# Optimization experiments

Hardware: AMD Instinct MI355X
Metric: run time of the kernel (lower is better)

The kernel has to match this reference:

```python
import jax, jax.numpy as jnp
import numpy as np

B, F, V, E = 16384, 39, 100000, 16
D0, D1, D2 = 32, 32, 32

def setup_inputs() -> dict:
    key = jax.random.key(0)
    ks = jax.random.split(key, 12)
    return {
        "Xi": jax.random.randint(ks[0], (B, F, 1), 0, V),
        "Xv": jax.random.uniform(ks[1], (B, F), dtype=jnp.float32),
        "emb_tables": jax.random.normal(ks[2], (F, V, E), dtype=jnp.float32),
        "w_first": jax.random.normal(ks[3], (D0, F, E), dtype=jnp.float32),
        "w_inner": jax.random.normal(ks[4], (D0, F, E), dtype=jnp.float32),
        "lin1_W": jax.random.normal(ks[5], (D1, D0), dtype=jnp.float32) * 0.1,
        "lin1_b": jax.random.normal(ks[6], (D1,), dtype=jnp.float32) * 0.1,
        "lin2_W": jax.random.normal(ks[7], (D2, D1), dtype=jnp.float32) * 0.1,
        "lin2_b": jax.random.normal(ks[8], (D2,), dtype=jnp.float32) * 0.1,
        "last_W": jax.random.normal(ks[9], (1, D2), dtype=jnp.float32) * 0.1,
        "last_b": jax.random.normal(ks[10], (1,), dtype=jnp.float32) * 0.1,
    }

def reference(Xi, Xv, emb_tables, w_first, w_inner, lin1_W, lin1_b, lin2_W, lin2_b, last_W, last_b):
    idx = Xi[:, :, 0]                                  # [B,F]
    # per-field embedding gather, scaled by feature value
    emb = emb_tables[jnp.arange(F)[None, :], idx]      # [B,F,E]
    emb = emb * Xv[:, :, None]                         # [B,F,E]
    # first-order: nested loops over (D0, F) collapse to one einsum
    first = jnp.einsum('bfe,dfe->bd', emb, w_first)    # [B,D0]
    # inner-product second-order: (sum over fields of <emb_f, w_df>)^2
    s = jnp.einsum('bfe,dfe->bd', emb, w_inner)        # [B,D0]
    x = first + s * s
    # deep MLP (relu, no dropout/batchnorm in inference)
    x = jax.nn.relu(x @ lin1_W.T + lin1_b)
    x = jax.nn.relu(x @ lin2_W.T + lin2_b)
    x = x @ last_W.T + last_b                          # [B,1]
    return jnp.sum(x, axis=1)                          # [B]
```

## Files before the change

### kernel.cpp

```cpp
#include <hip/hip_runtime.h>


namespace {

typedef _Float16 half8 __attribute__((ext_vector_type(8)));
typedef _Float16 half4 __attribute__((ext_vector_type(4)));
typedef float floatx4 __attribute__((ext_vector_type(4)));
typedef float f32x4 __attribute__((ext_vector_type(4)));

constexpr int Bn = 16384;
constexpr int Fn = 39;
constexpr int Vn = 100000;
constexpr int En = 16;
constexpr int M = 32;
constexpr int KST = 20;
constexpr int GITER = 10;
constexpr int NTOT = Bn * Fn;

constexpr int CHUNK_LOG = 11;
constexpr int CHUNK = 1 << CHUNK_LOG;
constexpr int NB = (Vn + CHUNK - 1) / CHUNK;
constexpr int NBUCKET = Fn * NB;
constexpr int CAP = 512;
constexpr int CUR_STRIDE = 16;

constexpr size_t OFF_CUR = 0;
constexpr size_t OFF_ENT = 131072;
constexpr size_t OFF_AEMB = 8388608;

__device__ __forceinline__ half8 cvt8(float4 a, float4 b) {
    half8 h;
    h[0] = (_Float16)a.x; h[1] = (_Float16)a.y;
    h[2] = (_Float16)a.z; h[3] = (_Float16)a.w;
    h[4] = (_Float16)b.x; h[5] = (_Float16)b.y;
    h[6] = (_Float16)b.z; h[7] = (_Float16)b.w;
    return h;
}

__device__ __forceinline__ half4 cvt4(f32x4 a) {
    half4 h;
    h[0] = (_Float16)a[0];
    h[1] = (_Float16)a[1];
    h[2] = (_Float16)a[2];
    h[3] = (_Float16)a[3];
    return h;
}

__global__ __launch_bounds__(256) void pnn_zero(unsigned int* __restrict__ cur)
{
    const int i = blockIdx.x * 256 + threadIdx.x;
    if (i < NBUCKET) cur[(size_t)i * CUR_STRIDE] = 0u;
}

__global__ __launch_bounds__(256) void pnn_bin(
    const int* __restrict__ Xi,
    const float* __restrict__ Xv,
    unsigned int* __restrict__ cur,
    uint2* __restrict__ ent)
{
    const int i = blockIdx.x * 256 + threadIdx.x;
    if (i >= NTOT) return;
    const unsigned int idx = (unsigned int)Xi[i];
    const float v = Xv[i];
    const unsigned int b = (unsigned int)i / (unsigned int)Fn;
    const unsigned int f = (unsigned int)i - b * (unsigned int)Fn;
    const unsigned int bucket = f * NB + (idx >> CHUNK_LOG);
    const unsigned int pos = atomicAdd(&cur[(size_t)bucket * CUR_STRIDE], 1u);
    if (pos < CAP) {
        uint2 e;
        e.x = b | ((idx & (unsigned int)(CHUNK - 1)) << 14);
        e.y = __float_as_uint(v);
        ent[(size_t)bucket * CAP + pos] = e;
    }
}

__global__ __launch_bounds__(256) void pnn_scatter(
    const float* __restrict__ T,
    const unsigned int* __restrict__ cur,
    const uint2* __restrict__ ent,
    float* __restrict__ Aemb)
{
    const int blk = blockIdx.x;
    const int f = blk / NB;
    const int ch = blk - f * NB;
    const int tid = threadIdx.x;

    unsigned int cnt = cur[(size_t)blk * CUR_STRIDE];
    if (cnt > CAP) cnt = CAP;
    const int ntask = (int)cnt * 4;

    const float* __restrict__ Tb =
        T + ((size_t)f * Vn + (size_t)ch * CHUNK) * En;
    const uint2* __restrict__ eb = ent + (size_t)blk * CAP;

    for (int g = 0; g < 2; ++g) {
        f32x4 v[4]; float s[4]; int c4[4]; unsigned int bb[4]; bool ok[4];
#pragma unroll
        for (int k = 0; k < 4; ++k) {
            const int task = tid + (g * 4 + k) * 256;
            ok[k] = task < ntask;
            if (ok[k]) {
                const uint2 e = eb[task >> 2];
                const int c = task & 3;
                bb[k] = e.x & 16383u;
                const unsigned int il = e.x >> 14;
                s[k] = __uint_as_float(e.y);
                c4[k] = c;
                v[k] = *reinterpret_cast<const f32x4*>(
                    Tb + (size_t)il * En + c * 4);
            }
        }
#pragma unroll
        for (int k = 0; k < 4; ++k) {
            if (ok[k]) {
                f32x4 r;
                r[0] = v[k][0] * s[k];
                r[1] = v[k][1] * s[k];
                r[2] = v[k][2] * s[k];
                r[3] = v[k][3] * s[k];
                *reinterpret_cast<f32x4*>(
                    Aemb + ((size_t)bb[k] * Fn + f) * En + c4[k] * 4) = r;
            }
        }
    }
}

struct SMemGather {
    _Float16 At[2][KST * 512];
};
struct SMemMlp {
    float x[M * 69];
    float wsh[2176];
    float r1[1024];
    float r2[1024];
};
union SMemU {
    SMemGather g;
    SMemMlp m;
};

__global__ __launch_bounds__(512, 4) void pnn_gemm(
    const float* __restrict__ Aemb,
    const float* __restrict__ w_first,
    const float* __restrict__ w_inner,
    const float* __restrict__ lin1_W,
    const float* __restrict__ lin1_b,
    const float* __restrict__ lin2_W,
    const float* __restrict__ lin2_b,
    const float* __restrict__ last_W,
    const float* __restrict__ last_b,
    float* __restrict__ out)
{
    __shared__ SMemU sm;

    const int tid = threadIdx.x;
    const int lane = tid & 63;
    const int wv = tid >> 6;
    const int q = wv & 1;
    const int t16 = wv >> 1;
    const int row0 = blockIdx.x * M;

    if (tid < 64) {
        half8 z = {0, 0, 0, 0, 0, 0, 0, 0};
        const int qq = tid >> 5;
        *reinterpret_cast<half8*>(
            &sm.g.At[qq][((KST - 1) * 64 + 32 + (tid & 31)) * 8]) = z;
    }

    f32x4 v[GITER];
    int   slot[GITER];
    bool  ok[GITER];
#pragma unroll
    for (int it = 0; it < GITER; ++it) {
        const int i = tid + it * 512;
        ok[it] = (i < M * Fn * 4);
        if (ok[it]) {
            const int j = i >> 2, c = i & 3;
            const int r = j & 31, f = j >> 5;
            v[it] = *reinterpret_cast<const f32x4*>(
                Aemb + ((size_t)(row0 + r) * Fn + f) * En + c * 4);
            slot[it] = (r >> 4) * (KST * 512)
                     + (((f >> 1) * 64) + (f & 1) * 32 + (r & 15)) * 8
                     + (c >> 1) * 128 + (c & 1) * 4;
        }
    }
#pragma unroll
    for (int it = 0; it < GITER; ++it) {
        if (ok[it])
            *reinterpret_cast<half4*>(&sm.g.At[0][0] + slot[it]) = cvt4(v[it]);
    }
    __syncthreads();

    const int n = t16 * 16 + (lane & 15);
    const int kq = lane >> 4;
    const float* wrow = (n < 32) ? (w_first + (size_t)n * 624)
                                 : (w_inner + (size_t)(n - 32) * 624);
    const _Float16* aLds = &sm.g.At[q][lane * 8];

    floatx4 acc = {0.0f, 0.0f, 0.0f, 0.0f};
#pragma unroll
    for (int t = 0; t < KST; ++t) {
        const half8 af = *reinterpret_cast<const half8*>(aLds + t * 512);
        half8 bf;
        if (t == KST - 1 && kq >= 2) {
            bf = half8{0, 0, 0, 0, 0, 0, 0, 0};
        } else {
            const int kb = t * 32 + kq * 8;
            const float4 a = *reinterpret_cast<const float4*>(wrow + kb);
            const float4 b = *reinterpret_cast<const float4*>(wrow + kb + 4);
            bf = cvt8(a, b);
        }
        acc = __builtin_amdgcn_mfma_f32_16x16x32_f16(af, bf, acc, 0, 0, 0);
    }

    __syncthreads();

    {
        const int col = t16 * 16 + (lane & 15);
        const int rbase = q * 16 + (lane >> 4) * 4;
#pragma unroll
        for (int r = 0; r < 4; ++r)
            sm.m.x[(rbase + r) * 69 + col] = acc[r];
    }

    for (int i = tid; i < 2145; i += 512) {
        float vv;
        if (i < 1024)      vv = lin1_W[i];
        else if (i < 2048) vv = lin2_W[i - 1024];
        else if (i < 2080) vv = lin1_b[i - 2048];
        else if (i < 2112) vv = lin2_b[i - 2080];
        else if (i < 2144) vv = last_W[i - 2112];
        else               vv = last_b[0];
        sm.m.wsh[i] = vv;
    }
    __syncthreads();

    for (int p = tid; p < 1024; p += 512) {
        const int j = p >> 5, r = p & 31;
        const float fi = sm.m.x[r * 69 + j];
        const float sq = sm.m.x[r * 69 + 32 + j];
        sm.m.r1[j * 32 + r] = fi + sq * sq;
    }
    __syncthreads();

    {
        const int r = tid & 31, n0 = (tid >> 5) * 2;
        float a0 = sm.m.wsh[2048 + n0];
        float a1 = sm.m.wsh[2048 + n0 + 1];
#pragma unroll
        for (int j = 0; j < 32; ++j) {
            const float xj = sm.m.r1[j * 32 + r];
            a0 = fmaf(sm.m.wsh[n0 * 32 + j],       xj, a0);
            a1 = fmaf(sm.m.wsh[(n0 + 1) * 32 + j], xj, a1);
        }
        sm.m.r2[n0 * 32 + r]       = fmaxf(a0, 0.0f);
        sm.m.r2[(n0 + 1) * 32 + r] = fmaxf(a1, 0.0f);
    }
    __syncthreads();

    {
        const int r = tid & 31, n0 = (tid >> 5) * 2;
        float a0 = sm.m.wsh[2080 + n0];
        float a1 = sm.m.wsh[2080 + n0 + 1];
#pragma unroll
        for (int j = 0; j < 32; ++j) {
            const float xj = sm.m.r2[j * 32 + r];
            a0 = fmaf(sm.m.wsh[1024 + n0 * 32 + j],       xj, a0);
            a1 = fmaf(sm.m.wsh[1024 + (n0 + 1) * 32 + j], xj, a1);
        }
        sm.m.r1[n0 * 32 + r]       = fmaxf(a0, 0.0f);
        sm.m.r1[(n0 + 1) * 32 + r] = fmaxf(a1, 0.0f);
    }
    __syncthreads();

    if (tid < M) {
        float res = sm.m.wsh[2144];
#pragma unroll
        for (int j = 0; j < 32; ++j)
            res = fmaf(sm.m.wsh[2112 + j], sm.m.r1[j * 32 + tid], res);
        out[row0 + tid] = res;
    }
}

}

extern "C" void kernel_launch(void* const* d_in, const int* in_sizes, int n_in,
                              void* d_out, int out_size, void* d_ws, size_t ws_size,
                              hipStream_t stream) {
    (void)in_sizes; (void)n_in; (void)out_size; (void)ws_size;
    const int*   Xi      = (const int*)d_in[0];
    const float* Xv      = (const float*)d_in[1];
    const float* T       = (const float*)d_in[2];
    const float* w_first = (const float*)d_in[3];
    const float* w_inner = (const float*)d_in[4];
    const float* lin1_W  = (const float*)d_in[5];
    const float* lin1_b  = (const float*)d_in[6];
    const float* lin2_W  = (const float*)d_in[7];
    const float* lin2_b  = (const float*)d_in[8];
    const float* last_W  = (const float*)d_in[9];
    const float* last_b  = (const float*)d_in[10];
    float* out = (float*)d_out;

    unsigned int* cur = (unsigned int*)((char*)d_ws + OFF_CUR);
    uint2*        ent = (uint2*)((char*)d_ws + OFF_ENT);
    float*        Aemb = (float*)((char*)d_ws + OFF_AEMB);

    hipLaunchKernelGGL(pnn_zero, dim3((NBUCKET + 255) / 256), dim3(256), 0, stream,
                       cur);
    hipLaunchKernelGGL(pnn_bin, dim3((NTOT + 255) / 256), dim3(256), 0, stream,
                       Xi, Xv, cur, ent);
    hipLaunchKernelGGL(pnn_scatter, dim3(NBUCKET), dim3(256), 0, stream,
                       T, cur, ent, Aemb);
    hipLaunchKernelGGL(pnn_gemm, dim3(Bn / M), dim3(512), 0, stream,
                       Aemb, w_first, w_inner,
                       lin1_W, lin1_b, lin2_W, lin2_b, last_W, last_b, out);
}
```

Baseline: 385.7 us.

## Stage each embedding table chunk in LDS before scaling selected rows

The scatter kernel becomes a select kernel with 512 threads. Each block first copies its whole 1024-row slice of the embedding table into shared memory with coalesced loads. It then serves every binned lookup from shared memory, scales it by the feature value and writes it to Aemb. The bucket chunk size is halved and the per-bucket capacity and workspace offsets change to match. The aim is to replace scattered 64-byte global gathers with streaming reads, but every block now reads the full chunk (the entire table overall) even though only a small fraction of rows is used, which greatly increases the bytes read.

```diff
diff --git a/kernel.cpp b/kernel.cpp
--- a/kernel.cpp
+++ b/kernel.cpp
@@ -17,16 +17,16 @@
 constexpr int GITER = 10;
 constexpr int NTOT = Bn * Fn;
 
-constexpr int CHUNK_LOG = 11;
+constexpr int CHUNK_LOG = 10;
 constexpr int CHUNK = 1 << CHUNK_LOG;
 constexpr int NB = (Vn + CHUNK - 1) / CHUNK;
 constexpr int NBUCKET = Fn * NB;
-constexpr int CAP = 512;
+constexpr int CAP = 320;
 constexpr int CUR_STRIDE = 16;
 
 constexpr size_t OFF_CUR = 0;
-constexpr size_t OFF_ENT = 131072;
-constexpr size_t OFF_AEMB = 8388608;
+constexpr size_t OFF_ENT = 262144;
+constexpr size_t OFF_AEMB = 16777216;
 
 __device__ __forceinline__ half8 cvt8(float4 a, float4 b) {
     half8 h;
@@ -74,54 +74,45 @@
     }
 }
 
-__global__ __launch_bounds__(256) void pnn_scatter(
+__global__ __launch_bounds__(512) void pnn_select(
     const float* __restrict__ T,
     const unsigned int* __restrict__ cur,
     const uint2* __restrict__ ent,
     float* __restrict__ Aemb)
 {
+    __shared__ float Lw[CHUNK * En];
     const int blk = blockIdx.x;
     const int f = blk / NB;
     const int ch = blk - f * NB;
     const int tid = threadIdx.x;
 
+    const int rows = min(CHUNK, Vn - ch * CHUNK);
+    const f32x4* __restrict__ T4 = reinterpret_cast<const f32x4*>(
+        T + ((size_t)f * Vn + (size_t)ch * CHUNK) * En);
+    f32x4* L4 = reinterpret_cast<f32x4*>(Lw);
+    const int nchunk = rows * 4;
+    for (int i = tid; i < nchunk; i += 512)
+        L4[i] = T4[i];
+    __syncthreads();
+
     unsigned int cnt = cur[(size_t)blk * CUR_STRIDE];
     if (cnt > CAP) cnt = CAP;
     const int ntask = (int)cnt * 4;
-
-    const float* __restrict__ Tb =
-        T + ((size_t)f * Vn + (size_t)ch * CHUNK) * En;
     const uint2* __restrict__ eb = ent + (size_t)blk * CAP;
-
-    for (int g = 0; g < 2; ++g) {
-        f32x4 v[4]; float s[4]; int c4[4]; unsigned int bb[4]; bool ok[4];
-#pragma unroll
-        for (int k = 0; k < 4; ++k) {
-            const int task = tid + (g * 4 + k) * 256;
-            ok[k] = task < ntask;
-            if (ok[k]) {
-                const uint2 e = eb[task >> 2];
-                const int c = task & 3;
-                bb[k] = e.x & 16383u;
-                const unsigned int il = e.x >> 14;
-                s[k] = __uint_as_float(e.y);
-                c4[k] = c;
-                v[k] = *reinterpret_cast<const f32x4*>(
-                    Tb + (size_t)il * En + c * 4);
-            }
-        }
-#pragma unroll
-        for (int k = 0; k < 4; ++k) {
-            if (ok[k]) {
-                f32x4 r;
-                r[0] = v[k][0] * s[k];
-                r[1] = v[k][1] * s[k];
-                r[2] = v[k][2] * s[k];
-                r[3] = v[k][3] * s[k];
-                *reinterpret_cast<f32x4*>(
-                    Aemb + ((size_t)bb[k] * Fn + f) * En + c4[k] * 4) = r;
-            }
-        }
+    for (int task = tid; task < ntask; task += 512) {
+        const uint2 e = eb[task >> 2];
+        const int c = task & 3;
+        const unsigned int b = e.x & 16383u;
+        const unsigned int il = e.x >> 14;
+        const float s = __uint_as_float(e.y);
+        const f32x4 v = L4[il * 4 + c];
+        f32x4 r;
+        r[0] = v[0] * s;
+        r[1] = v[1] * s;
+        r[2] = v[2] * s;
+        r[3] = v[3] * s;
+        *reinterpret_cast<f32x4*>(
+            Aemb + ((size_t)b * Fn + f) * En + c * 4) = r;
     }
 }
 
@@ -309,7 +300,7 @@
                        cur);
     hipLaunchKernelGGL(pnn_bin, dim3((NTOT + 255) / 256), dim3(256), 0, stream,
                        Xi, Xv, cur, ent);
-    hipLaunchKernelGGL(pnn_scatter, dim3(NBUCKET), dim3(256), 0, stream,
+    hipLaunchKernelGGL(pnn_select, dim3(NBUCKET), dim3(512), 0, stream,
                        T, cur, ent, Aemb);
     hipLaunchKernelGGL(pnn_gemm, dim3(Bn / M), dim3(512), 0, stream,
                        Aemb, w_first, w_inner,
```

Measured after the change: 420.7 us. 1.09x slower.
